# Optimization experiments

Hardware: AMD Instinct MI355X
Metric: run time of the kernel (lower is better)

Reference implementation:

```python
import jax, jax.numpy as jnp
import numpy as np
from jax import lax

DN = ('NCHW', 'OIHW', 'NCHW')
BN_EPS = 1e-5

def conv2d(x, w, b=None, pad=0):
    y = lax.conv_general_dilated(x, w, (1, 1), [(pad, pad), (pad, pad)], dimension_numbers=DN)
    if b is not None:
        y = y + b[None, :, None, None]
    return y

def setup_inputs() -> dict:
    key = jax.random.key(0)
    ks = jax.random.split(key, 12)
    B, C, H, W = 8, 256, 64, 64
    ca = C // 4  # dim_att = 64
    s = 0.05  # weight scale to keep attention logits sane
    return {
        'x': jax.random.normal(ks[0], (B, C, H, W), jnp.float32),
        'w_dw1': jax.random.normal(ks[1], (ca // 2, ca, 7, 7), jnp.float32) * s,
        'b_dw1': jax.random.normal(ks[2], (ca // 2,), jnp.float32) * s,
        'w_dw2': jax.random.normal(ks[3], (ca // 2, ca, 11, 11), jnp.float32) * s,
        'b_dw2': jax.random.normal(ks[4], (ca // 2,), jnp.float32) * s,
        'w_k': jax.random.normal(ks[5], (ca, ca, 1, 1), jnp.float32) * s,
        'b_k': jax.random.normal(ks[6], (ca,), jnp.float32) * s,
        'w_v': jax.random.normal(ks[7], (ca, ca, 1, 1), jnp.float32) * s,
        'b_v': jax.random.normal(ks[8], (ca,), jnp.float32) * s,
        'w_c1': jax.random.normal(ks[9], (C, C, 1, 1), jnp.float32) * s,
        'bn_g': jnp.ones((C,), jnp.float32),
        'bn_b': jnp.zeros((C,), jnp.float32),
        'bn_m': jnp.zeros((C,), jnp.float32),
        'bn_var': jnp.ones((C,), jnp.float32),
        'w_c2': jax.random.normal(ks[10], (C, C, 1, 1), jnp.float32) * s,
        'b_c2': jax.random.normal(ks[11], (C,), jnp.float32) * s,
    }

def reference(x, w_dw1, b_dw1, w_dw2, b_dw2, w_k, b_k, w_v, b_v,
              w_c1, bn_g, bn_b, bn_m, bn_var, w_c2, b_c2):
    ca = w_k.shape[0]  # dim_att
    B, C, H, W = x.shape
    HW = H * W
    x1 = x[:, :ca]
    x2 = x[:, ca:]
    # Q from two multi-scale convs (7x7 and 11x11, same padding)
    q = jnp.concatenate([conv2d(x1, w_dw1, b_dw1, pad=3),
                         conv2d(x1, w_dw2, b_dw2, pad=5)], axis=1)  # [B,ca,H,W]
    q = q.reshape(B, ca, HW)                                         # [B,ca,HW]
    k = conv2d(x1, w_k, b_k).reshape(B, ca, HW)                      # [B,ca,HW]
    v = conv2d(x1, w_v, b_v).reshape(B, ca, HW)                      # [B,ca,HW]
    # att[b,n,m] = softmax_m( sum_c q[b,c,n] * k[b,c,m] )
    att = jax.nn.softmax(jnp.einsum('bcn,bcm->bnm', q, k), axis=-1)  # [B,HW,HW]
    # out1[b,c,n] = sum_m v[b,c,m] * att[b,n,m]
    out1 = jnp.einsum('bcm,bnm->bcn', v, att).reshape(B, ca, H, W)
    y = jnp.concatenate([out1, x2], axis=1)  # [B,C,H,W]
    # conv1 = YOLO Conv: 1x1 conv (no bias) + BatchNorm (eval stats) + SiLU
    y = conv2d(y, w_c1)
    inv = lax.rsqrt(bn_var + BN_EPS)
    y = (y - bn_m[None, :, None, None]) * (bn_g * inv)[None, :, None, None] + bn_b[None, :, None, None]
    y = jax.nn.silu(y)
    # conv2 = plain 1x1 conv with bias
    return conv2d(y, w_c2, b_c2)
```

## Files before the change

### kernel.cpp

```cpp
#include <hip/hip_runtime.h>

typedef __attribute__((ext_vector_type(8))) short frag8;
typedef __attribute__((ext_vector_type(4))) float f32x4;
typedef __attribute__((ext_vector_type(8))) unsigned short us8;

#define MFMA(a,b,c) __builtin_amdgcn_mfma_f32_16x16x32_bf16((a),(b),(c),0,0,0)

__device__ __forceinline__ unsigned short f2bf(float f){
  unsigned int u = __builtin_bit_cast(unsigned int, f);
  u += 0x7fffu + ((u >> 16) & 1u);
  return (unsigned short)(u >> 16);
}

#define OFF_XT   ((size_t)0)
#define OFF_KT   ((size_t)16777216)
#define OFF_VCT  ((size_t)20971520)
#define OFF_QT   ((size_t)25165824)
#define OFF_O1T  ((size_t)29360128)
#define OFF_ZT   ((size_t)33554432)
#define OFF_WQ7  ((size_t)50331648)
#define OFF_WQ11 ((size_t)50532352)
#define OFF_WC1  ((size_t)51027968)
#define OFF_WC2  ((size_t)51159040)
#define OFF_BC1  ((size_t)51290112)
#define OFF_WKB  ((size_t)51291136)
#define OFF_WVB  ((size_t)51299328)
#define OFF_ML   OFF_WQ7

__global__ __launch_bounds__(256) void prep_weights_kernel(
    const float* __restrict__ wdw1, const float* __restrict__ wdw2,
    const float* __restrict__ wc1, const float* __restrict__ bng,
    const float* __restrict__ bnb, const float* __restrict__ bnm,
    const float* __restrict__ bnv, const float* __restrict__ wc2,
    const float* __restrict__ wk, const float* __restrict__ wv,
    unsigned short* __restrict__ wq7, unsigned short* __restrict__ wq11,
    unsigned short* __restrict__ wc1b, unsigned short* __restrict__ wc2b,
    float* __restrict__ bc1, unsigned short* __restrict__ wkb,
    unsigned short* __restrict__ wvb){
  int i = blockIdx.x*256 + threadIdx.x;
  if (i < 100352){
    int o = i >> 11, rem = i & 2047;
    int co = rem >> 6, ci = rem & 63;
    int kh = o / 7, kw = o % 7;
    wq7[i] = f2bf(wdw1[(co*64 + ci)*49 + kh*7 + kw]);
  } else if (i < 348160){
    int j = i - 100352;
    int o = j >> 11, rem = j & 2047;
    int co = rem >> 6, ci = rem & 63;
    int kh = o / 11, kw = o % 11;
    wq11[j] = f2bf(wdw2[(co*64 + ci)*121 + kh*11 + kw]);
  } else if (i < 413696){
    int j = i - 348160;
    int co = j >> 8;
    float a = bng[co] * rsqrtf(bnv[co] + 1e-5f);
    wc1b[j] = f2bf(wc1[j] * a);
    if ((j & 255) == 0) bc1[co] = bnb[co] - bnm[co]*a;
  } else if (i < 479232){
    int j = i - 413696;
    wc2b[j] = f2bf(wc2[j]);
  } else if (i < 483328){
    int j = i - 479232;
    wkb[j] = f2bf(wk[j]);
  } else if (i < 487424){
    int j = i - 483328;
    wvb[j] = f2bf(wv[j]);
  }
}

__global__ __launch_bounds__(256) void prep_x_kernel(const float* __restrict__ x,
                                                     unsigned short* __restrict__ xt){
  int g = blockIdx.x*256 + threadIdx.x;
  int b = g >> 12, n = g & 4095;
  int c0base = blockIdx.y * 64;
  const float* xp = x + (((size_t)b*256) << 12) + n;
  unsigned short* op = xt + (size_t)g*256;
  for (int c0 = c0base; c0 < c0base + 64; c0 += 8){
    us8 v;
    #pragma unroll
    for (int j = 0; j < 8; ++j) v[j] = f2bf(xp[(size_t)(c0+j) << 12]);
    *reinterpret_cast<us8*>(op + c0) = v;
  }
}

__global__ __launch_bounds__(256) void kv_kernel(const unsigned short* __restrict__ xt,
    const unsigned short* __restrict__ wkb, const unsigned short* __restrict__ wvb,
    const float* __restrict__ bk, const float* __restrict__ bv,
    unsigned short* __restrict__ kt, unsigned short* __restrict__ vct){
  int gid = blockIdx.x;
  int part = gid >> 9, t = gid & 511;
  int b = t >> 6, tile = t & 63;
  int lane = threadIdx.x & 63, wid = threadIdx.x >> 6;
  int lo = lane & 15, hi = lane >> 4;
  int n0 = tile*64 + wid*16;
  size_t bb = (size_t)b << 12;
  f32x4 acc[4];
  #pragma unroll
  for (int f = 0; f < 4; ++f) acc[f] = (f32x4){0.f,0.f,0.f,0.f};
  frag8 x0 = *reinterpret_cast<const frag8*>(xt + (bb + n0 + lo)*256 + 8*hi);
  frag8 x1 = *reinterpret_cast<const frag8*>(xt + (bb + n0 + lo)*256 + 32 + 8*hi);
  if (part == 0){
    #pragma unroll
    for (int nf = 0; nf < 4; ++nf){
      frag8 w0 = *reinterpret_cast<const frag8*>(wkb + (nf*16 + lo)*64 + 8*hi);
      frag8 w1 = *reinterpret_cast<const frag8*>(wkb + (nf*16 + lo)*64 + 32 + 8*hi);
      acc[nf] = MFMA(x0, w0, acc[nf]);
      acc[nf] = MFMA(x1, w1, acc[nf]);
    }
    #pragma unroll
    for (int nf = 0; nf < 4; ++nf){
      int co = nf*16 + lo;
      float bias = bk[co];
      #pragma unroll
      for (int r = 0; r < 4; ++r)
        kt[(bb + n0 + hi*4 + r)*64 + co] = f2bf(acc[nf][r] + bias);
    }
  } else {
    #pragma unroll
    for (int mf = 0; mf < 4; ++mf){
      frag8 w0 = *reinterpret_cast<const frag8*>(wvb + (mf*16 + lo)*64 + 8*hi);
      frag8 w1 = *reinterpret_cast<const frag8*>(wvb + (mf*16 + lo)*64 + 32 + 8*hi);
      acc[mf] = MFMA(w0, x0, acc[mf]);
      acc[mf] = MFMA(w1, x1, acc[mf]);
    }
    #pragma unroll
    for (int mf = 0; mf < 4; ++mf){
      #pragma unroll
      for (int r = 0; r < 4; ++r){
        int c = mf*16 + hi*4 + r;
        vct[(((size_t)b*64 + c) << 12) + n0 + lo] = f2bf(acc[mf][r] + bv[c]);
      }
    }
  }
}

template<int KS>
__global__ __launch_bounds__(256) void conv_q_kernel(const unsigned short* __restrict__ xt,
    const unsigned short* __restrict__ wq, const float* __restrict__ bias,
    unsigned short* __restrict__ qt){
  constexpr int P = KS/2;
  __shared__ unsigned short xs[(P+1)*64*64];
  __shared__ float outst[64*33];
  int h = blockIdx.x, b = blockIdx.y;
  int tid = threadIdx.x, lane = tid & 63, wid = tid >> 6;
  int lo = lane & 15, hi = lane >> 4;
  int cofrag = wid & 1, nhalf = wid >> 1;
  f32x4 acc[2] = {{0.f,0.f,0.f,0.f},{0.f,0.f,0.f,0.f}};
  const size_t xbase = ((size_t)b << 12) * 256;
  #pragma unroll
  for (int pass = 0; pass < 2; ++pass){
    const int nrows = pass ? P : (P+1);
    const int srcBase = pass ? (h+1) : (h-P);
    const int dhBase = pass ? (P+1) : 0;
    if (pass) __syncthreads();
    for (int idx = tid; idx < nrows*512; idx += 256){
      int rl = idx >> 9, w = (idx >> 3) & 63, ch = idx & 7;
      int sr = srcBase + rl;
      us8 v = {0,0,0,0,0,0,0,0};
      if (sr >= 0 && sr < 64)
        v = *reinterpret_cast<const us8*>(xt + xbase + (size_t)(sr*64 + w)*256 + ch*8);
      int byte = (rl*64 + w)*128 + ((ch*16) ^ ((w & 7) << 4));
      *reinterpret_cast<us8*>((char*)xs + byte) = v;
    }
    __syncthreads();
    for (int dh = 0; dh < nrows; ++dh){
      frag8 wf[KS][2];
      int off0 = (dhBase + dh)*KS;
      #pragma unroll
      for (int dw = 0; dw < KS; ++dw){
        #pragma unroll
        for (int ks = 0; ks < 2; ++ks)
          wf[dw][ks] = *reinterpret_cast<const frag8*>(
              wq + (size_t)(off0+dw)*2048 + (cofrag*16 + lo)*64 + ks*32 + 8*hi);
      }
      #pragma unroll
      for (int dw = 0; dw < KS; ++dw){
        #pragma unroll
        for (int nf = 0; nf < 2; ++nf){
          int w_out = nhalf*32 + nf*16 + lo;
          int wp = w_out + dw - P;
          frag8 bx0 = {0,0,0,0,0,0,0,0}, bx1 = {0,0,0,0,0,0,0,0};
          if (wp >= 0 && wp < 64){
            int rowb = (dh*64 + wp)*128;
            int sw = (wp & 7) << 4;
            bx0 = *reinterpret_cast<const frag8*>((char*)xs + rowb + ((hi*16) ^ sw));
            bx1 = *reinterpret_cast<const frag8*>((char*)xs + rowb + ((64 + hi*16) ^ sw));
          }
          acc[nf] = MFMA(wf[dw][0], bx0, acc[nf]);
          acc[nf] = MFMA(wf[dw][1], bx1, acc[nf]);
        }
      }
    }
  }
  __syncthreads();
  #pragma unroll
  for (int nf = 0; nf < 2; ++nf){
    int w = nhalf*32 + nf*16 + lo;
    #pragma unroll
    for (int r = 0; r < 4; ++r){
      int co = cofrag*16 + hi*4 + r;
      outst[w*33 + co] = acc[nf][r];
    }
  }
  __syncthreads();
  {
    int w = tid >> 2, c8 = (tid & 3)*8;
    int cobase = (KS == 7) ? 0 : 32;
    us8 v;
    #pragma unroll
    for (int j = 0; j < 8; ++j) v[j] = f2bf(outst[w*33 + c8 + j] + bias[c8 + j]);
    *reinterpret_cast<us8*>(qt + (((size_t)b << 12) + h*64 + w)*64 + cobase + c8) = v;
  }
}

__global__ __launch_bounds__(256, 4) void attn_kernel(const unsigned short* __restrict__ qt,
    const unsigned short* __restrict__ kt, const unsigned short* __restrict__ vct,
    float* __restrict__ opart, float* __restrict__ mlpart){
  __shared__ unsigned short kls[2][64*64];
  __shared__ unsigned short vls[2][64*64];
  __shared__ unsigned short pls[4][16*64];
  int b = blockIdx.y, qb = blockIdx.x * 64, half = blockIdx.z;
  int tid = threadIdx.x, lane = tid & 63, wid = tid >> 6;
  int lo = lane & 15, hi = lane >> 4;
  int q0 = qb + wid*16;
  const size_t bb = (size_t)b << 12;
  const int mtbase = half * 32;
  const int sm = tid >> 3, sch = tid & 7;
  const int dstA = sm*128 + ((sch*16) ^ ((sm & 7) << 4));
  const int dstB = dstA + 32*128;
  frag8 aq0 = *reinterpret_cast<const frag8*>(qt + (bb + q0 + lo)*64 + 8*hi);
  frag8 aq1 = *reinterpret_cast<const frag8*>(qt + (bb + q0 + lo)*64 + 32 + 8*hi);
  f32x4 o[4];
  #pragma unroll
  for (int f = 0; f < 4; ++f) o[f] = (f32x4){0.f,0.f,0.f,0.f};
  float mr[4] = {-1e30f,-1e30f,-1e30f,-1e30f};
  float lr[4] = {0.f,0.f,0.f,0.f};
  us8 kr0, kr1, vr0, vr1;
  {
    int mt = mtbase;
    kr0 = *reinterpret_cast<const us8*>(kt + (bb + mt*64 + sm)*64 + sch*8);
    kr1 = *reinterpret_cast<const us8*>(kt + (bb + mt*64 + sm + 32)*64 + sch*8);
    vr0 = *reinterpret_cast<const us8*>(vct + (((size_t)b*64 + sm) << 12) + mt*64 + sch*8);
    vr1 = *reinterpret_cast<const us8*>(vct + (((size_t)b*64 + sm + 32) << 12) + mt*64 + sch*8);
    *reinterpret_cast<us8*>((char*)kls[0] + dstA) = kr0;
    *reinterpret_cast<us8*>((char*)kls[0] + dstB) = kr1;
    *reinterpret_cast<us8*>((char*)vls[0] + dstA) = vr0;
    *reinterpret_cast<us8*>((char*)vls[0] + dstB) = vr1;
  }
  __syncthreads();
  int cur = 0;
  for (int t = 0; t < 32; ++t){
    if (t < 31){
      int mt = mtbase + t + 1;
      kr0 = *reinterpret_cast<const us8*>(kt + (bb + mt*64 + sm)*64 + sch*8);
      kr1 = *reinterpret_cast<const us8*>(kt + (bb + mt*64 + sm + 32)*64 + sch*8);
      vr0 = *reinterpret_cast<const us8*>(vct + (((size_t)b*64 + sm) << 12) + mt*64 + sch*8);
      vr1 = *reinterpret_cast<const us8*>(vct + (((size_t)b*64 + sm + 32) << 12) + mt*64 + sch*8);
    }
    f32x4 s[4];
    #pragma unroll
    for (int f = 0; f < 4; ++f) s[f] = (f32x4){0.f,0.f,0.f,0.f};
    #pragma unroll
    for (int nf = 0; nf < 4; ++nf){
      int m = nf*16 + lo;
      int sw = (m & 7) << 4;
      frag8 b0 = *reinterpret_cast<const frag8*>((char*)kls[cur] + m*128 + ((hi*16) ^ sw));
      s[nf] = MFMA(aq0, b0, s[nf]);
      frag8 b1 = *reinterpret_cast<const frag8*>((char*)kls[cur] + m*128 + ((64 + hi*16) ^ sw));
      s[nf] = MFMA(aq1, b1, s[nf]);
    }
    float pm[4];
    #pragma unroll
    for (int r = 0; r < 4; ++r)
      pm[r] = fmaxf(fmaxf(s[0][r], s[1][r]), fmaxf(s[2][r], s[3][r]));
    float growth = fmaxf(fmaxf(pm[0]-mr[0], pm[1]-mr[1]),
                         fmaxf(pm[2]-mr[2], pm[3]-mr[3]));
    if (!__all(growth <= 8.0f)){
      float rmax[4] = {pm[0], pm[1], pm[2], pm[3]};
      #pragma unroll
      for (int msk = 1; msk < 16; msk <<= 1){
        #pragma unroll
        for (int r = 0; r < 4; ++r) rmax[r] = fmaxf(rmax[r], __shfl_xor(rmax[r], msk));
      }
      #pragma unroll
      for (int r = 0; r < 4; ++r){
        float mn = fmaxf(mr[r], rmax[r]);
        float sc = __expf(mr[r] - mn);
        mr[r] = mn;
        lr[r] *= sc;
        #pragma unroll
        for (int nf = 0; nf < 4; ++nf) o[nf][r] *= sc;
      }
    }
    #pragma unroll
    for (int nf = 0; nf < 4; ++nf){
      #pragma unroll
      for (int r = 0; r < 4; ++r) s[nf][r] = __expf(s[nf][r] - mr[r]);
    }
    #pragma unroll
    for (int r = 0; r < 4; ++r)
      lr[r] += (s[0][r] + s[1][r]) + (s[2][r] + s[3][r]);
    #pragma unroll
    for (int nf = 0; nf < 4; ++nf){
      #pragma unroll
      for (int r = 0; r < 4; ++r){
        int q = hi*4 + r, m = nf*16 + lo;
        *reinterpret_cast<unsigned short*>((char*)pls[wid] + q*128 + ((m*2) ^ ((q & 7) << 4)))
            = f2bf(s[nf][r]);
      }
    }
    #pragma unroll
    for (int ks = 0; ks < 2; ++ks){
      frag8 ap = *reinterpret_cast<const frag8*>(
          (char*)pls[wid] + lo*128 + ((ks*64 + hi*16) ^ ((lo & 7) << 4)));
      #pragma unroll
      for (int nf = 0; nf < 4; ++nf){
        int c = nf*16 + lo;
        frag8 bv = *reinterpret_cast<const frag8*>(
            (char*)vls[cur] + c*128 + ((ks*64 + hi*16) ^ ((c & 7) << 4)));
        o[nf] = MFMA(ap, bv, o[nf]);
      }
    }
    if (t < 31){
      *reinterpret_cast<us8*>((char*)kls[cur^1] + dstA) = kr0;
      *reinterpret_cast<us8*>((char*)kls[cur^1] + dstB) = kr1;
      *reinterpret_cast<us8*>((char*)vls[cur^1] + dstA) = vr0;
      *reinterpret_cast<us8*>((char*)vls[cur^1] + dstB) = vr1;
    }
    __syncthreads();
    cur ^= 1;
  }
  #pragma unroll
  for (int msk = 1; msk < 16; msk <<= 1){
    #pragma unroll
    for (int r = 0; r < 4; ++r) lr[r] += __shfl_xor(lr[r], msk);
  }
  size_t pb = ((size_t)(half*8 + b) << 12);
  #pragma unroll
  for (int nf = 0; nf < 4; ++nf){
    #pragma unroll
    for (int r = 0; r < 4; ++r)
      opart[(pb + q0 + hi*4 + r)*64 + nf*16 + lo] = o[nf][r];
  }
  if (lo == 0){
    #pragma unroll
    for (int r = 0; r < 4; ++r){
      size_t idx = pb + q0 + hi*4 + r;
      mlpart[idx*2]     = mr[r];
      mlpart[idx*2 + 1] = lr[r];
    }
  }
}

__global__ __launch_bounds__(256) void merge_kernel(const float* __restrict__ opart,
    const float* __restrict__ mlpart, unsigned short* __restrict__ o1t){
  int g = blockIdx.x*256 + threadIdx.x;
  int c4 = g & 15, q = (g >> 4) & 4095, b = g >> 16;
  size_t i0 = ((size_t)b << 12) + q;
  size_t i1 = ((size_t)(8 + b) << 12) + q;
  float m0 = mlpart[i0*2], l0 = mlpart[i0*2 + 1];
  float m1 = mlpart[i1*2], l1 = mlpart[i1*2 + 1];
  float M = fmaxf(m0, m1);
  float w0 = __expf(m0 - M), w1 = __expf(m1 - M);
  float inv = 1.0f / (w0*l0 + w1*l1);
  w0 *= inv; w1 *= inv;
  f32x4 a = *reinterpret_cast<const f32x4*>(opart + i0*64 + c4*4);
  f32x4 c = *reinterpret_cast<const f32x4*>(opart + i1*64 + c4*4);
  unsigned short outv[4];
  #pragma unroll
  for (int j = 0; j < 4; ++j) outv[j] = f2bf(w0*a[j] + w1*c[j]);
  *reinterpret_cast<ulonglong1*>(o1t + i0*64 + c4*4) =
      *reinterpret_cast<ulonglong1*>(outv);
}

__global__ __launch_bounds__(256) void c1_kernel(const unsigned short* __restrict__ o1t,
    const unsigned short* __restrict__ xt, const unsigned short* __restrict__ wc1b,
    const float* __restrict__ bc1, unsigned short* __restrict__ zt){
  int b = blockIdx.y;
  int q0 = blockIdx.x*64 + (threadIdx.x >> 6)*16;
  int lane = threadIdx.x & 63, lo = lane & 15, hi = lane >> 4;
  size_t bb = (size_t)b << 12;
  f32x4 acc[16];
  #pragma unroll
  for (int nf = 0; nf < 16; ++nf) acc[nf] = (f32x4){0.f,0.f,0.f,0.f};
  #pragma unroll
  for (int ks = 0; ks < 8; ++ks){
    int ci0 = ks*32 + 8*hi;
    frag8 a;
    if (ks < 2) a = *reinterpret_cast<const frag8*>(o1t + (bb + q0 + lo)*64 + ci0);
    else        a = *reinterpret_cast<const frag8*>(xt  + (bb + q0 + lo)*256 + ci0);
    #pragma unroll
    for (int nf = 0; nf < 16; ++nf){
      frag8 w = *reinterpret_cast<const frag8*>(wc1b + (nf*16 + lo)*256 + ci0);
      acc[nf] = MFMA(a, w, acc[nf]);
    }
  }
  #pragma unroll
  for (int nf = 0; nf < 16; ++nf){
    int co = nf*16 + lo;
    float bias = bc1[co];
    #pragma unroll
    for (int r = 0; r < 4; ++r){
      float y = acc[nf][r] + bias;
      y = y / (1.0f + __expf(-y));
      zt[(bb + q0 + hi*4 + r)*256 + co] = f2bf(y);
    }
  }
}

__global__ __launch_bounds__(256) void c2_kernel(const unsigned short* __restrict__ zt,
    const unsigned short* __restrict__ wc2b, const float* __restrict__ bc2,
    float* __restrict__ out){
  int b = blockIdx.y;
  int q0 = blockIdx.x*128 + (threadIdx.x >> 6)*32;
  int lane = threadIdx.x & 63, lo = lane & 15, hi = lane >> 4;
  size_t bb = (size_t)b << 12;
  f32x4 acc[16][2];
  #pragma unroll
  for (int mf = 0; mf < 16; ++mf){
    acc[mf][0] = (f32x4){0.f,0.f,0.f,0.f};
    acc[mf][1] = (f32x4){0.f,0.f,0.f,0.f};
  }
  #pragma unroll
  for (int ks = 0; ks < 8; ++ks){
    int ci0 = ks*32 + 8*hi;
    frag8 bz0 = *reinterpret_cast<const frag8*>(zt + (bb + q0 + lo)*256 + ci0);
    frag8 bz1 = *reinterpret_cast<const frag8*>(zt + (bb + q0 + 16 + lo)*256 + ci0);
    #pragma unroll
    for (int mf = 0; mf < 16; ++mf){
      frag8 aw = *reinterpret_cast<const frag8*>(wc2b + (mf*16 + lo)*256 + ci0);
      acc[mf][0] = MFMA(aw, bz0, acc[mf][0]);
      acc[mf][1] = MFMA(aw, bz1, acc[mf][1]);
    }
  }
  #pragma unroll
  for (int mf = 0; mf < 16; ++mf){
    #pragma unroll
    for (int r = 0; r < 4; ++r){
      int co = mf*16 + hi*4 + r;
      float bias = bc2[co];
      float* op = out + (((size_t)b*256 + co) << 12) + q0 + lo;
      op[0]  = acc[mf][0][r] + bias;
      op[16] = acc[mf][1][r] + bias;
    }
  }
}

extern "C" void kernel_launch(void* const* d_in, const int* in_sizes, int n_in,
                              void* d_out, int out_size, void* d_ws, size_t ws_size,
                              hipStream_t stream){
  const float* x    = (const float*)d_in[0];
  const float* wdw1 = (const float*)d_in[1];
  const float* bdw1 = (const float*)d_in[2];
  const float* wdw2 = (const float*)d_in[3];
  const float* bdw2 = (const float*)d_in[4];
  const float* wk   = (const float*)d_in[5];
  const float* bk   = (const float*)d_in[6];
  const float* wv   = (const float*)d_in[7];
  const float* bv   = (const float*)d_in[8];
  const float* wc1  = (const float*)d_in[9];
  const float* bng  = (const float*)d_in[10];
  const float* bnb  = (const float*)d_in[11];
  const float* bnm  = (const float*)d_in[12];
  const float* bnv  = (const float*)d_in[13];
  const float* wc2  = (const float*)d_in[14];
  const float* bc2  = (const float*)d_in[15];
  char* ws = (char*)d_ws;
  unsigned short* xt   = (unsigned short*)(ws + OFF_XT);
  unsigned short* ktp  = (unsigned short*)(ws + OFF_KT);
  unsigned short* vct  = (unsigned short*)(ws + OFF_VCT);
  unsigned short* qtp  = (unsigned short*)(ws + OFF_QT);
  unsigned short* o1t  = (unsigned short*)(ws + OFF_O1T);
  unsigned short* zt   = (unsigned short*)(ws + OFF_ZT);
  unsigned short* wq7  = (unsigned short*)(ws + OFF_WQ7);
  unsigned short* wq11 = (unsigned short*)(ws + OFF_WQ11);
  unsigned short* wc1b = (unsigned short*)(ws + OFF_WC1);
  unsigned short* wc2b = (unsigned short*)(ws + OFF_WC2);
  float*          bc1  = (float*)(ws + OFF_BC1);
  unsigned short* wkb  = (unsigned short*)(ws + OFF_WKB);
  unsigned short* wvb  = (unsigned short*)(ws + OFF_WVB);
  float*          opart = (float*)(ws + OFF_ZT);
  float*          mlp   = (float*)(ws + OFF_ML);

  prep_weights_kernel<<<1904, 256, 0, stream>>>(wdw1, wdw2, wc1, bng, bnb, bnm, bnv,
                                                wc2, wk, wv, wq7, wq11, wc1b, wc2b,
                                                bc1, wkb, wvb);
  prep_x_kernel<<<dim3(128, 4), 256, 0, stream>>>(x, xt);
  kv_kernel<<<1024, 256, 0, stream>>>(xt, wkb, wvb, bk, bv, ktp, vct);
  conv_q_kernel<7><<<dim3(64, 8), 256, 0, stream>>>(xt, wq7, bdw1, qtp);
  conv_q_kernel<11><<<dim3(64, 8), 256, 0, stream>>>(xt, wq11, bdw2, qtp);
  attn_kernel<<<dim3(64, 8, 2), 256, 0, stream>>>(qtp, ktp, vct, opart, mlp);
  merge_kernel<<<2048, 256, 0, stream>>>(opart, mlp, o1t);
  c1_kernel<<<dim3(64, 8), 256, 0, stream>>>(o1t, xt, wc1b, bc1, zt);
  c2_kernel<<<dim3(32, 8), 256, 0, stream>>>(zt, wc2b, bc2, (float*)d_out);
}
```

Before: 273.8 us.

## Process 32 query rows per wave in attention with transposed S tile

```diff
diff --git a/kernel.cpp b/kernel.cpp
--- a/kernel.cpp
+++ b/kernel.cpp
@@ -3,6 +3,7 @@
 typedef __attribute__((ext_vector_type(8))) short frag8;
 typedef __attribute__((ext_vector_type(4))) float f32x4;
 typedef __attribute__((ext_vector_type(8))) unsigned short us8;
+typedef __attribute__((ext_vector_type(2))) unsigned int u32x2;
 
 #define MFMA(a,b,c) __builtin_amdgcn_mfma_f32_16x16x32_bf16((a),(b),(c),0,0,0)
 
@@ -10,6 +11,12 @@
   unsigned int u = __builtin_bit_cast(unsigned int, f);
   u += 0x7fffu + ((u >> 16) & 1u);
   return (unsigned short)(u >> 16);
+}
+
+__device__ __forceinline__ unsigned int cvt_pk_bf16(float a, float b){
+  unsigned int r;
+  asm volatile("v_cvt_pk_bf16_f32 %0, %1, %2" : "=v"(r) : "v"(a), "v"(b));
+  return r;
 }
 
 #define OFF_XT   ((size_t)0)
@@ -212,28 +219,41 @@
   }
 }
 
-__global__ __launch_bounds__(256, 4) void attn_kernel(const unsigned short* __restrict__ qt,
+__global__ __launch_bounds__(256, 2) void attn_kernel(const unsigned short* __restrict__ qt,
     const unsigned short* __restrict__ kt, const unsigned short* __restrict__ vct,
     float* __restrict__ opart, float* __restrict__ mlpart){
   __shared__ unsigned short kls[2][64*64];
   __shared__ unsigned short vls[2][64*64];
-  __shared__ unsigned short pls[4][16*64];
-  int b = blockIdx.y, qb = blockIdx.x * 64, half = blockIdx.z;
+  __shared__ unsigned short pls[4][32*64];
+  int b = blockIdx.y, half = blockIdx.z;
   int tid = threadIdx.x, lane = tid & 63, wid = tid >> 6;
   int lo = lane & 15, hi = lane >> 4;
-  int q0 = qb + wid*16;
+  int q0 = blockIdx.x*128 + wid*32;
   const size_t bb = (size_t)b << 12;
   const int mtbase = half * 32;
   const int sm = tid >> 3, sch = tid & 7;
   const int dstA = sm*128 + ((sch*16) ^ ((sm & 7) << 4));
   const int dstB = dstA + 32*128;
-  frag8 aq0 = *reinterpret_cast<const frag8*>(qt + (bb + q0 + lo)*64 + 8*hi);
-  frag8 aq1 = *reinterpret_cast<const frag8*>(qt + (bb + q0 + lo)*64 + 32 + 8*hi);
-  f32x4 o[4];
-  #pragma unroll
-  for (int f = 0; f < 4; ++f) o[f] = (f32x4){0.f,0.f,0.f,0.f};
-  float mr[4] = {-1e30f,-1e30f,-1e30f,-1e30f};
-  float lr[4] = {0.f,0.f,0.f,0.f};
+  char* pbase = (char*)pls[wid];
+  frag8 aq[2][2];
+  #pragma unroll
+  for (int mf = 0; mf < 2; ++mf)
+    #pragma unroll
+    for (int ks = 0; ks < 2; ++ks)
+      aq[mf][ks] = *reinterpret_cast<const frag8*>(
+          qt + (bb + q0 + mf*16 + lo)*64 + ks*32 + 8*hi);
+  f32x4 o[2][4];
+  #pragma unroll
+  for (int mf = 0; mf < 2; ++mf)
+    #pragma unroll
+    for (int f = 0; f < 4; ++f) o[mf][f] = (f32x4){0.f,0.f,0.f,0.f};
+  float mr[2]  = {-1e30f, -1e30f};
+  float lr[2]  = {0.f, 0.f};
+  float mrT[2][4];
+  #pragma unroll
+  for (int mf = 0; mf < 2; ++mf)
+    #pragma unroll
+    for (int r = 0; r < 4; ++r) mrT[mf][r] = -1e30f;
   us8 kr0, kr1, vr0, vr1;
   {
     int mt = mtbase;
@@ -256,68 +276,84 @@
       vr0 = *reinterpret_cast<const us8*>(vct + (((size_t)b*64 + sm) << 12) + mt*64 + sch*8);
       vr1 = *reinterpret_cast<const us8*>(vct + (((size_t)b*64 + sm + 32) << 12) + mt*64 + sch*8);
     }
-    f32x4 s[4];
-    #pragma unroll
-    for (int f = 0; f < 4; ++f) s[f] = (f32x4){0.f,0.f,0.f,0.f};
+    f32x4 s[2][4];
+    #pragma unroll
+    for (int mf = 0; mf < 2; ++mf)
+      #pragma unroll
+      for (int f = 0; f < 4; ++f) s[mf][f] = (f32x4){0.f,0.f,0.f,0.f};
     #pragma unroll
     for (int nf = 0; nf < 4; ++nf){
       int m = nf*16 + lo;
       int sw = (m & 7) << 4;
       frag8 b0 = *reinterpret_cast<const frag8*>((char*)kls[cur] + m*128 + ((hi*16) ^ sw));
-      s[nf] = MFMA(aq0, b0, s[nf]);
       frag8 b1 = *reinterpret_cast<const frag8*>((char*)kls[cur] + m*128 + ((64 + hi*16) ^ sw));
-      s[nf] = MFMA(aq1, b1, s[nf]);
-    }
-    float pm[4];
-    #pragma unroll
-    for (int r = 0; r < 4; ++r)
-      pm[r] = fmaxf(fmaxf(s[0][r], s[1][r]), fmaxf(s[2][r], s[3][r]));
-    float growth = fmaxf(fmaxf(pm[0]-mr[0], pm[1]-mr[1]),
-                         fmaxf(pm[2]-mr[2], pm[3]-mr[3]));
+      s[0][nf] = MFMA(b0, aq[0][0], s[0][nf]);
+      s[0][nf] = MFMA(b1, aq[0][1], s[0][nf]);
+      s[1][nf] = MFMA(b0, aq[1][0], s[1][nf]);
+      s[1][nf] = MFMA(b1, aq[1][1], s[1][nf]);
+    }
+    float pm[2];
+    #pragma unroll
+    for (int mf = 0; mf < 2; ++mf){
+      float a0 = fmaxf(fmaxf(s[mf][0][0], s[mf][0][1]), fmaxf(s[mf][0][2], s[mf][0][3]));
+      float a1 = fmaxf(fmaxf(s[mf][1][0], s[mf][1][1]), fmaxf(s[mf][1][2], s[mf][1][3]));
+      float a2 = fmaxf(fmaxf(s[mf][2][0], s[mf][2][1]), fmaxf(s[mf][2][2], s[mf][2][3]));
+      float a3 = fmaxf(fmaxf(s[mf][3][0], s[mf][3][1]), fmaxf(s[mf][3][2], s[mf][3][3]));
+      pm[mf] = fmaxf(fmaxf(a0, a1), fmaxf(a2, a3));
+    }
+    float growth = fmaxf(pm[0] - mr[0], pm[1] - mr[1]);
     if (!__all(growth <= 8.0f)){
-      float rmax[4] = {pm[0], pm[1], pm[2], pm[3]};
-      #pragma unroll
-      for (int msk = 1; msk < 16; msk <<= 1){
+      float rmax[2] = {pm[0], pm[1]};
+      #pragma unroll
+      for (int mf = 0; mf < 2; ++mf){
+        rmax[mf] = fmaxf(rmax[mf], __shfl_xor(rmax[mf], 16));
+        rmax[mf] = fmaxf(rmax[mf], __shfl_xor(rmax[mf], 32));
+        float mn = fmaxf(mr[mf], rmax[mf]);
+        lr[mf] *= __expf(mr[mf] - mn);
+        mr[mf] = mn;
+      }
+      #pragma unroll
+      for (int mf = 0; mf < 2; ++mf)
         #pragma unroll
-        for (int r = 0; r < 4; ++r) rmax[r] = fmaxf(rmax[r], __shfl_xor(rmax[r], msk));
+        for (int r = 0; r < 4; ++r){
+          float mnT = __shfl(mr[mf], hi*4 + r);
+          float scT = __expf(mrT[mf][r] - mnT);
+          mrT[mf][r] = mnT;
+          #pragma unroll
+          for (int nf = 0; nf < 4; ++nf) o[mf][nf][r] *= scT;
+        }
+    }
+    #pragma unroll
+    for (int mf = 0; mf < 2; ++mf){
+      float acc = 0.f;
+      #pragma unroll
+      for (int nf = 0; nf < 4; ++nf){
+        #pragma unroll
+        for (int r = 0; r < 4; ++r){
+          s[mf][nf][r] = __expf(s[mf][nf][r] - mr[mf]);
+          acc += s[mf][nf][r];
+        }
+        u32x2 w;
+        w[0] = cvt_pk_bf16(s[mf][nf][0], s[mf][nf][1]);
+        w[1] = cvt_pk_bf16(s[mf][nf][2], s[mf][nf][3]);
+        *reinterpret_cast<u32x2*>(pbase + (mf*16 + lo)*128 +
+            ((nf*32 + hi*8) ^ ((lo & 7) << 4))) = w;
       }
-      #pragma unroll
-      for (int r = 0; r < 4; ++r){
-        float mn = fmaxf(mr[r], rmax[r]);
-        float sc = __expf(mr[r] - mn);
-        mr[r] = mn;
-        lr[r] *= sc;
-        #pragma unroll
-        for (int nf = 0; nf < 4; ++nf) o[nf][r] *= sc;
-      }
-    }
-    #pragma unroll
-    for (int nf = 0; nf < 4; ++nf){
-      #pragma unroll
-      for (int r = 0; r < 4; ++r) s[nf][r] = __expf(s[nf][r] - mr[r]);
-    }
-    #pragma unroll
-    for (int r = 0; r < 4; ++r)
-      lr[r] += (s[0][r] + s[1][r]) + (s[2][r] + s[3][r]);
-    #pragma unroll
-    for (int nf = 0; nf < 4; ++nf){
-      #pragma unroll
-      for (int r = 0; r < 4; ++r){
-        int q = hi*4 + r, m = nf*16 + lo;
-        *reinterpret_cast<unsigned short*>((char*)pls[wid] + q*128 + ((m*2) ^ ((q & 7) << 4)))
-            = f2bf(s[nf][r]);
-      }
+      lr[mf] += acc;
     }
     #pragma unroll
     for (int ks = 0; ks < 2; ++ks){
-      frag8 ap = *reinterpret_cast<const frag8*>(
-          (char*)pls[wid] + lo*128 + ((ks*64 + hi*16) ^ ((lo & 7) << 4)));
+      frag8 ap0 = *reinterpret_cast<const frag8*>(
+          pbase + lo*128 + ((ks*64 + hi*16) ^ ((lo & 7) << 4)));
+      frag8 ap1 = *reinterpret_cast<const frag8*>(
+          pbase + (16 + lo)*128 + ((ks*64 + hi*16) ^ ((lo & 7) << 4)));
       #pragma unroll
       for (int nf = 0; nf < 4; ++nf){
         int c = nf*16 + lo;
         frag8 bv = *reinterpret_cast<const frag8*>(
             (char*)vls[cur] + c*128 + ((ks*64 + hi*16) ^ ((c & 7) << 4)));
-        o[nf] = MFMA(ap, bv, o[nf]);
+        o[0][nf] = MFMA(ap0, bv, o[0][nf]);
+        o[1][nf] = MFMA(ap1, bv, o[1][nf]);
       }
     }
     if (t < 31){
@@ -330,23 +366,22 @@
     cur ^= 1;
   }
   #pragma unroll
-  for (int msk = 1; msk < 16; msk <<= 1){
-    #pragma unroll
-    for (int r = 0; r < 4; ++r) lr[r] += __shfl_xor(lr[r], msk);
+  for (int mf = 0; mf < 2; ++mf){
+    lr[mf] += __shfl_xor(lr[mf], 16);
+    lr[mf] += __shfl_xor(lr[mf], 32);
   }
   size_t pb = ((size_t)(half*8 + b) << 12);
   #pragma unroll
-  for (int nf = 0; nf < 4; ++nf){
-    #pragma unroll
-    for (int r = 0; r < 4; ++r)
-      opart[(pb + q0 + hi*4 + r)*64 + nf*16 + lo] = o[nf][r];
-  }
-  if (lo == 0){
-    #pragma unroll
-    for (int r = 0; r < 4; ++r){
-      size_t idx = pb + q0 + hi*4 + r;
-      mlpart[idx*2]     = mr[r];
-      mlpart[idx*2 + 1] = lr[r];
+  for (int mf = 0; mf < 2; ++mf){
+    #pragma unroll
+    for (int nf = 0; nf < 4; ++nf)
+      #pragma unroll
+      for (int r = 0; r < 4; ++r)
+        opart[(pb + q0 + mf*16 + hi*4 + r)*64 + nf*16 + lo] = o[mf][nf][r];
+    if (hi == 0){
+      size_t idx = pb + q0 + mf*16 + lo;
+      mlpart[idx*2]     = mr[mf];
+      mlpart[idx*2 + 1] = lr[mf];
     }
   }
 }
@@ -488,7 +523,7 @@
   kv_kernel<<<1024, 256, 0, stream>>>(xt, wkb, wvb, bk, bv, ktp, vct);
   conv_q_kernel<7><<<dim3(64, 8), 256, 0, stream>>>(xt, wq7, bdw1, qtp);
   conv_q_kernel<11><<<dim3(64, 8), 256, 0, stream>>>(xt, wq11, bdw2, qtp);
-  attn_kernel<<<dim3(64, 8, 2), 256, 0, stream>>>(qtp, ktp, vct, opart, mlp);
+  attn_kernel<<<dim3(32, 8, 2), 256, 0, stream>>>(qtp, ktp, vct, opart, mlp);
   merge_kernel<<<2048, 256, 0, stream>>>(opart, mlp, o1t);
   c1_kernel<<<dim3(64, 8), 256, 0, stream>>>(o1t, xt, wc1b, bc1, zt);
   c2_kernel<<<dim3(32, 8), 256, 0, stream>>>(zt, wc2b, bc2, (float*)d_out);
```

New measurement: 262.7 us. 1.04x faster.
